# Optimization experiments

Measured on AMD Instinct MI355X. Metric: run time of the kernel, lower is better.

The kernel has to match this reference:

```python
import jax, jax.numpy as jnp
import numpy as np

DIM = 1024
HEADS = 16
HEAD_DIM = DIM // HEADS
HIDDEN = int(DIM * 4.0)
EPS = 1e-5


def layernorm(x, w, b):
    m = jnp.mean(x, axis=-1, keepdims=True)
    v = jnp.var(x, axis=-1, keepdims=True)
    return (x - m) * jax.lax.rsqrt(v + EPS) * w + b


def apply_rope(t, pos):
    # t: [B, H, S, D], pos: [B, S] int
    half = t.shape[-1] // 2
    inv_freq = 1.0 / (10000.0 ** (jnp.arange(half, dtype=jnp.float32) / half))
    ang = pos.astype(jnp.float32)[:, None, :, None] * inv_freq  # [B,1,S,half]
    cos = jnp.cos(ang)
    sin = jnp.sin(ang)
    t1, t2 = t[..., :half], t[..., half:]
    return jnp.concatenate([t1 * cos - t2 * sin, t2 * cos + t1 * sin], axis=-1)


def setup_inputs() -> dict:
    key = jax.random.key(0)
    ks = jax.random.split(key, 10)
    B, S = 2, 2048
    x = jax.random.normal(ks[0], (B, S, DIM), dtype=jnp.float32)
    pos = jnp.sort(jax.random.randint(ks[1], (B, S), 0, 2048), axis=-1).astype(jnp.int32)
    def lin(k, fi, fo):
        return jax.random.normal(k, (fi, fo), dtype=jnp.float32) / np.sqrt(fi)
    return {
        "x": x,
        "pos": pos,
        "ln1_w": jnp.ones((DIM,), jnp.float32),
        "ln1_b": jnp.zeros((DIM,), jnp.float32),
        "qkv_w": lin(ks[2], DIM, 3 * DIM),
        "qkv_b": jnp.zeros((3 * DIM,), jnp.float32),
        "o_w": lin(ks[3], DIM, DIM),
        "o_b": jnp.zeros((DIM,), jnp.float32),
        "ln2_w": jnp.ones((DIM,), jnp.float32),
        "ln2_b": jnp.zeros((DIM,), jnp.float32),
        "mlp_w1": lin(ks[4], DIM, HIDDEN),
        "mlp_b1": jnp.zeros((HIDDEN,), jnp.float32),
        "mlp_w2": lin(ks[5], HIDDEN, DIM),
        "mlp_b2": jnp.zeros((DIM,), jnp.float32),
    }


def reference(x, pos, ln1_w, ln1_b, qkv_w, qkv_b, o_w, o_b, ln2_w, ln2_b, mlp_w1, mlp_b1, mlp_w2, mlp_b2):
    B, S, C = x.shape
    scale = HEAD_DIM ** -0.5
    xn = layernorm(x, ln1_w, ln1_b)
    qkv = (xn @ qkv_w + qkv_b).reshape(B, S, 3, HEADS, HEAD_DIM)
    qkv = jnp.transpose(qkv, (2, 0, 3, 1, 4))  # [3,B,H,S,D]
    q, k, v = qkv[0], qkv[1], qkv[2]
    q = apply_rope(q, pos)
    k = apply_rope(k, pos)
    scores = jnp.einsum("bhsd,bhtd->bhst", q, k) * scale
    probs = jax.nn.softmax(scores, axis=-1)
    attn = jnp.einsum("bhst,bhtd->bhsd", probs, v)
    attn = jnp.transpose(attn, (0, 2, 1, 3)).reshape(B, S, C)
    x = x + attn @ o_w + o_b
    xn2 = layernorm(x, ln2_w, ln2_b)
    h = jax.nn.gelu(xn2 @ mlp_w1 + mlp_b1, approximate=False)
    x = x + h @ mlp_w2 + mlp_b2
    return x
```

## Files before the change

### kernel.cpp

```cpp
#include <hip/hip_runtime.h>
#include <hip/hip_bf16.h>
#include <math.h>

#define DIMC 1024
#define HEADS 16
#define HD 64
#define HIDDEN 4096
#define BATCH 2
#define SEQ 2048
#define TOK (BATCH*SEQ)

typedef unsigned short u16;
typedef __attribute__((ext_vector_type(8))) short short8;
typedef __attribute__((ext_vector_type(4))) float f32x4;

__device__ __forceinline__ u16 f2bf(float f) {
  unsigned u = __float_as_uint(f);
  u += 0x7fff + ((u >> 16) & 1);
  return (u16)(u >> 16);
}
__device__ __forceinline__ float bf2f(u16 h) {
  return __uint_as_float(((unsigned)h) << 16);
}

__device__ __forceinline__ void gl_lds16(const void* g, void* l) {
  __builtin_amdgcn_global_load_lds(
      (__attribute__((address_space(1))) void*)g,
      (__attribute__((address_space(3))) void*)l, 16, 0, 0);
}

__device__ __forceinline__ const short8* lds_row128(const u16* base, int row, int chunk) {
  return (const short8*)((const char*)base + row * 128 + (((chunk) ^ (row & 7)) << 4));
}

__global__ __launch_bounds__(256) void ln_kernel(
    const float* __restrict__ x, const float* __restrict__ w,
    const float* __restrict__ b, u16* __restrict__ out)
{
  int row = blockIdx.x, tid = threadIdx.x;
  const float4* xr = (const float4*)(x + (size_t)row * DIMC);
  float4 v = xr[tid];
  float s = v.x + v.y + v.z + v.w;
  float s2 = v.x*v.x + v.y*v.y + v.z*v.z + v.w*v.w;
  for (int off = 32; off > 0; off >>= 1) {
    s  += __shfl_down(s, off);
    s2 += __shfl_down(s2, off);
  }
  __shared__ float red[8];
  int lane = tid & 63, wv = tid >> 6;
  if (lane == 0) { red[wv] = s; red[4 + wv] = s2; }
  __syncthreads();
  float S  = red[0] + red[1] + red[2] + red[3];
  float S2 = red[4] + red[5] + red[6] + red[7];
  float mean = S * (1.f / DIMC);
  float var  = S2 * (1.f / DIMC) - mean * mean;
  float inv  = rsqrtf(var + 1e-5f);
  int base = tid * 4;
  float vv[4] = {v.x, v.y, v.z, v.w};
#pragma unroll
  for (int j = 0; j < 4; ++j)
    out[(size_t)row * DIMC + base + j] = f2bf((vv[j] - mean) * inv * w[base + j] + b[base + j]);
}

__global__ __launch_bounds__(256) void transpose_cast(
    const float* __restrict__ W, u16* __restrict__ Wt, int K, int N)
{
  __shared__ float t[32][33];
  int n0 = blockIdx.x * 32, k0 = blockIdx.y * 32;
  for (int r = threadIdx.y; r < 32; r += 8)
    t[r][threadIdx.x] = W[(size_t)(k0 + r) * N + n0 + threadIdx.x];
  __syncthreads();
  for (int r = threadIdx.y; r < 32; r += 8)
    Wt[(size_t)(n0 + r) * K + k0 + threadIdx.x] = f2bf(t[threadIdx.x][r]);
}

template<int EPI, int BM>
__global__ __launch_bounds__(256) void gemm_bt(
    const u16* __restrict__ A, const u16* __restrict__ Bt,
    const float* __restrict__ bias, const float* __restrict__ res,
    u16* __restrict__ outb, float* __restrict__ outf,
    int M, int N, int K)
{
  constexpr int AMM = BM / 32;
  constexpr int HALF = BM / 2;
  __shared__ u16 shm[(BM + 128) * 32 * 2];
  u16* As[2] = { shm,             shm + BM * 32 };
  u16* Bs[2] = { shm + 2 * BM * 32, shm + 2 * BM * 32 + 128 * 32 };
  int tid = threadIdx.x;
  int lane = tid & 63, w = tid >> 6;
  int wr = w >> 1, wc = w & 1;

  int nwg = gridDim.x * gridDim.y;
  int orig = blockIdx.y * gridDim.x + blockIdx.x;
  int wg = (orig & 7) * (nwg >> 3) + (orig >> 3);
  int gi = wg >> 4, wi = wg & 15;
  int gx4 = gridDim.x >> 2;
  int bx = (gi % gx4) * 4 + (wi & 3);
  int by = (gi / gx4) * 4 + (wi >> 2);
  int m0 = by * BM, n0 = bx * 128;

  f32x4 acc[AMM][4] = {};

  int trow = tid >> 2;
  int tk = (((tid & 3) ^ ((tid >> 3) & 3)) * 8);
  const u16* ga = A  + (size_t)(m0 + trow) * K + tk;
  const u16* gb = Bt + (size_t)(n0 + trow) * K + tk;
  int rofs = lane & 15, q4 = lane >> 4;
  int ach = ((q4 ^ ((rofs >> 1) & 3)) << 4);
  int nt = K >> 5;

  auto stage = [&](int buf) {
    gl_lds16(ga, As[buf] + tid * 8);
    if (BM == 128) gl_lds16(ga + (size_t)64 * K, As[buf] + tid * 8 + 2048);
    gl_lds16(gb, Bs[buf] + tid * 8);
    gl_lds16(gb + (size_t)64 * K, Bs[buf] + tid * 8 + 2048);
    ga += 32; gb += 32;
  };
  auto compute = [&](int buf) {
    short8 af[AMM], bfr[4];
#pragma unroll
    for (int mm = 0; mm < AMM; ++mm)
      af[mm] = *(const short8*)((const char*)As[buf] + (wr * HALF + mm * 16 + rofs) * 64 + ach);
#pragma unroll
    for (int nn = 0; nn < 4; ++nn)
      bfr[nn] = *(const short8*)((const char*)Bs[buf] + (wc * 64 + nn * 16 + rofs) * 64 + ach);
#pragma unroll
    for (int mm = 0; mm < AMM; ++mm)
#pragma unroll
      for (int nn = 0; nn < 4; ++nn)
        acc[mm][nn] = __builtin_amdgcn_mfma_f32_16x16x32_bf16(af[mm], bfr[nn], acc[mm][nn], 0, 0, 0);
  };

  stage(0);
  __syncthreads();
  for (int t = 0; t < nt; t += 2) {
    if (t + 1 < nt) stage(1);
    compute(0);
    __syncthreads();
    if (t + 2 < nt) stage(0);
    compute(1);
    __syncthreads();
  }

  if (EPI == 0 || EPI == 1) {
    u16* C = shm;
#pragma unroll
    for (int nn = 0; nn < 4; ++nn) {
      int ccol = wc * 64 + nn * 16 + rofs;
      float bv = bias[n0 + ccol];
#pragma unroll
      for (int mm = 0; mm < AMM; ++mm)
#pragma unroll
        for (int r = 0; r < 4; ++r) {
          int crow = wr * HALF + mm * 16 + q4 * 4 + r;
          float v = acc[mm][nn][r] + bv;
          if (EPI == 1) v = 0.5f * v * (1.f + erff(v * 0.70710678118f));
          C[crow * 128 + ccol] = f2bf(v);
        }
    }
    __syncthreads();
    for (int c = tid; c < BM * 16; c += 256) {
      int row = c >> 4, off = (c & 15) * 8;
      *(short8*)(outb + (size_t)(m0 + row) * N + n0 + off) = *(const short8*)&C[row * 128 + off];
    }
  } else {
    float* Cf = (float*)shm;
#pragma unroll
    for (int p = 0; p < 2; ++p) {
      if (wr == p) {
#pragma unroll
        for (int nn = 0; nn < 4; ++nn) {
          int ccol = wc * 64 + nn * 16 + rofs;
          float bv = bias[n0 + ccol];
#pragma unroll
          for (int mm = 0; mm < AMM; ++mm)
#pragma unroll
            for (int r = 0; r < 4; ++r)
              Cf[(mm * 16 + q4 * 4 + r) * 128 + ccol] = acc[mm][nn][r] + bv;
        }
      }
      __syncthreads();
      for (int c = tid; c < HALF * 32; c += 256) {
        int row = c >> 5, off = (c & 31) * 4;
        size_t idx = (size_t)(m0 + p * HALF + row) * N + n0 + off;
        float4 rv = *(const float4*)(res + idx);
        float4 cv = *(const float4*)&Cf[row * 128 + off];
        cv.x += rv.x; cv.y += rv.y; cv.z += rv.z; cv.w += rv.w;
        *(float4*)(outf + idx) = cv;
      }
      __syncthreads();
    }
  }
}

__global__ __launch_bounds__(256) void rope_split(
    const u16* __restrict__ qkv, const int* __restrict__ pos,
    u16* __restrict__ Q, u16* __restrict__ Kk, u16* __restrict__ Vt)
{
  int st = blockIdx.x, bh = blockIdx.y;
  int b = bh >> 4, hh = bh & 15;
  int s0 = st * 64;
  int tid = threadIdx.x;
  __shared__ u16 vtile[64][72];

  for (int i = tid; i < 64 * 32; i += 256) {
    int sl = i >> 5, dp = i & 31;
    int s = s0 + sl;
    float p = (float)pos[b * SEQ + s];
    float freq = exp2f((float)dp * -0.4152410118609203f);
    float ang = p * freq;
    float sn, c;
    __sincosf(ang, &sn, &c);
    const u16* qr = qkv + (size_t)(b * SEQ + s) * 3072 + hh * 64;
    float q1 = bf2f(qr[dp]),        q2 = bf2f(qr[dp + 32]);
    float k1 = bf2f(qr[1024 + dp]), k2 = bf2f(qr[1024 + dp + 32]);
    size_t ob = ((size_t)bh * SEQ + s) * HD;
    const float QS = 0.18033688011112042f;
    Q[ob + dp]       = f2bf((q1 * c - q2 * sn) * QS);
    Q[ob + dp + 32]  = f2bf((q2 * c + q1 * sn) * QS);
    Kk[ob + dp]      = f2bf(k1 * c - k2 * sn);
    Kk[ob + dp + 32] = f2bf(k2 * c + k1 * sn);
  }
  for (int i = tid; i < 64 * 64; i += 256) {
    int sl = i >> 6, d = i & 63;
    vtile[d][sl] = qkv[(size_t)(b * SEQ + s0 + sl) * 3072 + 2048 + hh * 64 + d];
  }
  __syncthreads();
  for (int i = tid; i < 64 * 64; i += 256) {
    int d = i >> 6, sl = i & 63;
    Vt[((size_t)bh * HD + d) * SEQ + s0 + sl] = vtile[d][sl];
  }
}

__global__ __launch_bounds__(256) void attn_kernel(
    const u16* __restrict__ Q, const u16* __restrict__ K,
    const u16* __restrict__ Vt, u16* __restrict__ O)
{
  __shared__ u16 Ks[2][64 * 64];
  __shared__ u16 Vs[2][64 * 64];
  __shared__ u16 Ps[4 * 16 * 64];
  int qt = blockIdx.x, bh = blockIdx.y;
  int b = bh >> 4, hh = bh & 15;
  const u16* Qp = Q + ((size_t)bh * SEQ + qt * 64) * HD;
  const u16* Kp = K + (size_t)bh * SEQ * HD;
  const u16* Vp = Vt + (size_t)bh * HD * SEQ;
  int tid = threadIdx.x, lane = tid & 63, w = tid >> 6;
  int rofs = lane & 15, q4 = lane >> 4;
  int kofs = q4 * 8;

  short8 aq0 = *(const short8*)&Qp[(w * 16 + rofs) * HD + kofs];
  short8 aq1 = *(const short8*)&Qp[(w * 16 + rofs) * HD + 32 + kofs];

  short8 ones;
#pragma unroll
  for (int j = 0; j < 8; ++j) ones[j] = (short)0x3F80;

  f32x4 o[4] = {};
  f32x4 lsum = {};

  int srow = tid >> 3;
  int sg0 = ((tid & 7) ^ (srow & 7)) * 8;
  u16* pw = &Ps[w * 16 * 64];

#define A_STAGE(BUF, T0) do { \
    gl_lds16(Kp + (size_t)((T0) + srow) * HD + sg0, &Ks[BUF][tid * 8]); \
    gl_lds16(Kp + (size_t)((T0) + 32 + srow) * HD + sg0, &Ks[BUF][tid * 8 + 2048]); \
    gl_lds16(Vp + (size_t)srow * SEQ + (T0) + sg0, &Vs[BUF][tid * 8]); \
    gl_lds16(Vp + (size_t)(32 + srow) * SEQ + (T0) + sg0, &Vs[BUF][tid * 8 + 2048]); \
  } while (0)

  auto tile = [&](const u16* KsB, const u16* VsB) {
    f32x4 s[4] = {};
#pragma unroll
    for (int n = 0; n < 4; ++n) {
      int krow = n * 16 + rofs;
      short8 bk0 = *lds_row128(KsB, krow, q4);
      short8 bk1 = *lds_row128(KsB, krow, 4 + q4);
      s[n] = __builtin_amdgcn_mfma_f32_16x16x32_bf16(aq0, bk0, s[n], 0, 0, 0);
      s[n] = __builtin_amdgcn_mfma_f32_16x16x32_bf16(aq1, bk1, s[n], 0, 0, 0);
    }
#pragma unroll
    for (int n = 0; n < 4; ++n)
#pragma unroll
      for (int r = 0; r < 4; ++r) {
        int prow = q4 * 4 + r;
        int pbyte = (n * 16 + rofs) * 2;
        float p = __builtin_amdgcn_exp2f(s[n][r]);
        *(u16*)((char*)pw + prow * 128 + (pbyte ^ ((prow & 7) << 4))) = f2bf(p);
      }
    short8 pa0 = *lds_row128(pw, rofs, q4);
    short8 pa1 = *lds_row128(pw, rofs, 4 + q4);
    lsum = __builtin_amdgcn_mfma_f32_16x16x32_bf16(pa0, ones, lsum, 0, 0, 0);
    lsum = __builtin_amdgcn_mfma_f32_16x16x32_bf16(pa1, ones, lsum, 0, 0, 0);
#pragma unroll
    for (int n = 0; n < 4; ++n) {
      int vrow = n * 16 + rofs;
      short8 bv0 = *lds_row128(VsB, vrow, q4);
      short8 bv1 = *lds_row128(VsB, vrow, 4 + q4);
      o[n] = __builtin_amdgcn_mfma_f32_16x16x32_bf16(pa0, bv0, o[n], 0, 0, 0);
      o[n] = __builtin_amdgcn_mfma_f32_16x16x32_bf16(pa1, bv1, o[n], 0, 0, 0);
    }
  };

  A_STAGE(0, 0);
  __syncthreads();
  for (int t0 = 0; t0 < SEQ; t0 += 128) {
    if (t0 + 64 < SEQ) A_STAGE(1, t0 + 64);
    tile(Ks[0], Vs[0]);
    __syncthreads();
    if (t0 + 128 < SEQ) A_STAGE(0, t0 + 128);
    tile(Ks[1], Vs[1]);
    __syncthreads();
  }
#undef A_STAGE

#pragma unroll
  for (int r = 0; r < 4; ++r) {
    float inv = 1.f / lsum[r];
    int lrow = w * 16 + q4 * 4 + r;
#pragma unroll
    for (int n = 0; n < 4; ++n)
      Ps[lrow * 64 + n * 16 + rofs] = f2bf(o[n][r] * inv);
  }
  __syncthreads();
  for (int c = tid; c < 512; c += 256) {
    int row = c >> 3, off = (c & 7) * 8;
    int sq = qt * 64 + row;
    *(short8*)(O + ((size_t)b * SEQ + sq) * DIMC + hh * 64 + off) = *(const short8*)&Ps[row * 64 + off];
  }
}

extern "C" void kernel_launch(void* const* d_in, const int* in_sizes, int n_in,
                              void* d_out, int out_size, void* d_ws, size_t ws_size,
                              hipStream_t stream) {
  const float* x     = (const float*)d_in[0];
  const int*   pos   = (const int*)  d_in[1];
  const float* ln1_w = (const float*)d_in[2];
  const float* ln1_b = (const float*)d_in[3];
  const float* qkv_w = (const float*)d_in[4];
  const float* qkv_b = (const float*)d_in[5];
  const float* o_w   = (const float*)d_in[6];
  const float* o_b   = (const float*)d_in[7];
  const float* ln2_w = (const float*)d_in[8];
  const float* ln2_b = (const float*)d_in[9];
  const float* w1    = (const float*)d_in[10];
  const float* b1    = (const float*)d_in[11];
  const float* w2    = (const float*)d_in[12];
  const float* b2    = (const float*)d_in[13];
  float* out = (float*)d_out;

  char* ws = (char*)d_ws;
  u16* WqkvT = (u16*)(ws + 0);
  u16* WoT   = (u16*)(ws + 6291456);
  u16* W1T   = (u16*)(ws + 8388608);
  u16* W2T   = (u16*)(ws + 16777216);
  u16* xn    = (u16*)(ws + 25165824);
  u16* qkvbf = (u16*)(ws + 33554432);
  u16* Qb    = (u16*)(ws + 58720256);
  u16* Kb    = (u16*)(ws + 67108864);
  u16* Vtb   = (u16*)(ws + 75497472);
  u16* attnb = (u16*)(ws + 83886080);
  u16* hbuf  = (u16*)(ws + 25165824);
  float* x2  = (float*)(ws + 58720256);
  u16* xn2   = (u16*)(ws + 75497472);

  transpose_cast<<<dim3(3072/32, 1024/32), dim3(32, 8), 0, stream>>>(qkv_w, WqkvT, 1024, 3072);
  transpose_cast<<<dim3(1024/32, 1024/32), dim3(32, 8), 0, stream>>>(o_w,  WoT,  1024, 1024);
  transpose_cast<<<dim3(4096/32, 1024/32), dim3(32, 8), 0, stream>>>(w1,   W1T,  1024, 4096);
  transpose_cast<<<dim3(1024/32, 4096/32), dim3(32, 8), 0, stream>>>(w2,   W2T,  4096, 1024);

  ln_kernel<<<TOK, 256, 0, stream>>>(x, ln1_w, ln1_b, xn);
  gemm_bt<0,128><<<dim3(24, 32), 256, 0, stream>>>(xn, WqkvT, qkv_b, nullptr, qkvbf, nullptr, 4096, 3072, 1024);
  rope_split<<<dim3(32, 32), 256, 0, stream>>>(qkvbf, pos, Qb, Kb, Vtb);
  attn_kernel<<<dim3(32, 32), 256, 0, stream>>>(Qb, Kb, Vtb, attnb);
  gemm_bt<2,64><<<dim3(8, 64), 256, 0, stream>>>(attnb, WoT, o_b, x, nullptr, x2, 4096, 1024, 1024);
  ln_kernel<<<TOK, 256, 0, stream>>>(x2, ln2_w, ln2_b, xn2);
  gemm_bt<1,128><<<dim3(32, 32), 256, 0, stream>>>(xn2, W1T, b1, nullptr, hbuf, nullptr, 4096, 4096, 1024);
  gemm_bt<2,64><<<dim3(8, 64), 256, 0, stream>>>(hbuf, W2T, b2, x2, nullptr, out, 4096, 1024, 4096);
}
```

Before: 268.3 us.

## Add 256x256-tile MFMA GEMM with swizzled LDS and grouped scheduling for QKV and MLP1

Adds a new 512-thread GEMM kernel with 256x256 output tiles, K-step 64, XOR-swizzled LDS staging loaded directly from global memory, and double buffering. It remaps workgroup IDs into 4x4 groups to improve L2 reuse, and stages the output through LDS for coalesced stores. It replaces the 128-row-tile GEMMs for the QKV projection and the first MLP layer. The larger tiles raise arithmetic intensity. In exchange, the grids shrink to 192 and 256 blocks, and the 128KB of LDS per block limits occupancy.

New measurement: 280.6 us. +4.6%, slower.

```diff
diff --git a/kernel.cpp b/kernel.cpp
--- a/kernel.cpp
+++ b/kernel.cpp
@@ -72,6 +72,116 @@
   __syncthreads();
   for (int r = threadIdx.y; r < 32; r += 8)
     Wt[(size_t)(n0 + r) * K + k0 + threadIdx.x] = f2bf(t[threadIdx.x][r]);
+}
+
+template<int EPI>
+__global__ __launch_bounds__(512, 2) void gemm256(
+    const u16* __restrict__ A, const u16* __restrict__ Bt,
+    const float* __restrict__ bias, u16* __restrict__ outb,
+    int M, int N, int K)
+{
+  __shared__ u16 AB[2][2][256 * 64];
+  int tid = threadIdx.x;
+  int lane = tid & 63, wid = tid >> 6;
+  int wr = wid >> 2, wn = wid & 3;
+  int rofs = lane & 15, q4 = lane >> 4;
+
+  int nwg = gridDim.x * gridDim.y;
+  int orig = blockIdx.y * gridDim.x + blockIdx.x;
+  int wg = (orig & 7) * (nwg >> 3) + (orig >> 3);
+  int gi = wg >> 4, wi = wg & 15;
+  int gx4 = gridDim.x >> 2;
+  int bx = (gi % gx4) * 4 + (wi & 3);
+  int by = (gi / gx4) * 4 + (wi >> 2);
+  int m0 = by * 256, n0 = bx * 256;
+  int mb = wr * 128, nb = wn * 64;
+
+  f32x4 acc[8][4] = {};
+
+  int off[4];
+#pragma unroll
+  for (int j = 0; j < 4; ++j) {
+    int p = tid + j * 512;
+    int row = p >> 3;
+    int cl = (p & 7) ^ (row & 7);
+    off[j] = row * K + cl * 8;
+  }
+  const u16* gA = A  + (size_t)m0 * K;
+  const u16* gB = Bt + (size_t)n0 * K;
+
+  auto stage = [&](int b, int t) {
+#pragma unroll
+    for (int j = 0; j < 4; ++j) {
+      int p8 = (tid + j * 512) * 8;
+      gl_lds16(gA + off[j] + t * 64, &AB[b][0][p8]);
+      gl_lds16(gB + off[j] + t * 64, &AB[b][1][p8]);
+    }
+  };
+  auto comp = [&](int b) {
+    const char* Ab = (const char*)&AB[b][0][0];
+    const char* Bb = (const char*)&AB[b][1][0];
+    short8 bf[4][2];
+#pragma unroll
+    for (int nn = 0; nn < 4; ++nn)
+#pragma unroll
+      for (int kk = 0; kk < 2; ++kk) {
+        int row = nb + nn * 16 + rofs;
+        bf[nn][kk] = *(const short8*)(Bb + row * 128 + ((((kk << 2) | q4) ^ (row & 7)) << 4));
+      }
+#pragma unroll
+    for (int mg = 0; mg < 2; ++mg) {
+      short8 af[4][2];
+#pragma unroll
+      for (int mm = 0; mm < 4; ++mm)
+#pragma unroll
+        for (int kk = 0; kk < 2; ++kk) {
+          int row = mb + (mg * 4 + mm) * 16 + rofs;
+          af[mm][kk] = *(const short8*)(Ab + row * 128 + ((((kk << 2) | q4) ^ (row & 7)) << 4));
+        }
+      __builtin_amdgcn_s_setprio(1);
+#pragma unroll
+      for (int kk = 0; kk < 2; ++kk)
+#pragma unroll
+        for (int mm = 0; mm < 4; ++mm)
+#pragma unroll
+          for (int nn = 0; nn < 4; ++nn)
+            acc[mg * 4 + mm][nn] = __builtin_amdgcn_mfma_f32_16x16x32_bf16(
+                af[mm][kk], bf[nn][kk], acc[mg * 4 + mm][nn], 0, 0, 0);
+      __builtin_amdgcn_s_setprio(0);
+    }
+  };
+
+  int NT = K >> 6;
+  stage(0, 0);
+  __syncthreads();
+  int cur = 0;
+  for (int t = 0; t < NT; ++t) {
+    if (t + 1 < NT) stage(cur ^ 1, t + 1);
+    comp(cur);
+    __syncthreads();
+    cur ^= 1;
+  }
+
+  u16* Ct = &AB[0][0][0];
+#pragma unroll
+  for (int nn = 0; nn < 4; ++nn) {
+    int ccol = nb + nn * 16 + rofs;
+    float bv = bias[n0 + ccol];
+#pragma unroll
+    for (int m = 0; m < 8; ++m)
+#pragma unroll
+      for (int r = 0; r < 4; ++r) {
+        int row = mb + m * 16 + q4 * 4 + r;
+        float v = acc[m][nn][r] + bv;
+        if (EPI == 1) v = 0.5f * v * (1.f + erff(v * 0.70710678118f));
+        Ct[row * 256 + ccol] = f2bf(v);
+      }
+  }
+  __syncthreads();
+  for (int c = tid; c < 256 * 32; c += 512) {
+    int row = c >> 5, offb = (c & 31) * 8;
+    *(short8*)(outb + (size_t)(m0 + row) * N + n0 + offb) = *(const short8*)&Ct[row * 256 + offb];
+  }
 }
 
 template<int EPI, int BM>
@@ -370,11 +480,11 @@
   transpose_cast<<<dim3(1024/32, 4096/32), dim3(32, 8), 0, stream>>>(w2,   W2T,  4096, 1024);
 
   ln_kernel<<<TOK, 256, 0, stream>>>(x, ln1_w, ln1_b, xn);
-  gemm_bt<0,128><<<dim3(24, 32), 256, 0, stream>>>(xn, WqkvT, qkv_b, nullptr, qkvbf, nullptr, 4096, 3072, 1024);
+  gemm256<0><<<dim3(12, 16), 512, 0, stream>>>(xn, WqkvT, qkv_b, qkvbf, 4096, 3072, 1024);
   rope_split<<<dim3(32, 32), 256, 0, stream>>>(qkvbf, pos, Qb, Kb, Vtb);
   attn_kernel<<<dim3(32, 32), 256, 0, stream>>>(Qb, Kb, Vtb, attnb);
   gemm_bt<2,64><<<dim3(8, 64), 256, 0, stream>>>(attnb, WoT, o_b, x, nullptr, x2, 4096, 1024, 1024);
   ln_kernel<<<TOK, 256, 0, stream>>>(x2, ln2_w, ln2_b, xn2);
-  gemm_bt<1,128><<<dim3(32, 32), 256, 0, stream>>>(xn2, W1T, b1, nullptr, hbuf, nullptr, 4096, 4096, 1024);
+  gemm256<1><<<dim3(16, 16), 512, 0, stream>>>(xn2, W1T, b1, hbuf, 4096, 4096, 1024);
   gemm_bt<2,64><<<dim3(8, 64), 256, 0, stream>>>(hbuf, W2T, b2, x2, nullptr, out, 4096, 1024, 4096);
 }
```

## Double GEMM K-tile to 64 with 8-chunk XOR swizzle and precomputed offsets

Applied to the files above, without the earlier changes.

The GEMM main loop now stages 64-wide K tiles instead of 32, which halves the number of barrier-separated iterations and doubles the MFMA work between synchronizations. The LDS layout changes to 128-byte rows with an XOR swizzle over 8 chunks, and global load offsets are precomputed per thread. This doubles LDS usage per block, which may reduce occupancy. Offsets are kept as int, which is fine for these sizes.

Result: faster. 256.6 us (-4.3%).

```diff
diff --git a/kernel.cpp b/kernel.cpp
--- a/kernel.cpp
+++ b/kernel.cpp
@@ -81,11 +81,12 @@
     u16* __restrict__ outb, float* __restrict__ outf,
     int M, int N, int K)
 {
-  constexpr int AMM = BM / 32;
+  constexpr int AMM  = BM / 32;
   constexpr int HALF = BM / 2;
-  __shared__ u16 shm[(BM + 128) * 32 * 2];
-  u16* As[2] = { shm,             shm + BM * 32 };
-  u16* Bs[2] = { shm + 2 * BM * 32, shm + 2 * BM * 32 + 128 * 32 };
+  constexpr int AJ   = BM / 32;
+  constexpr int ASZ  = BM * 64;
+  constexpr int BSZ  = 128 * 64;
+  __shared__ u16 shm[(BM + 128) * 64 * 2];
   int tid = threadIdx.x;
   int lane = tid & 63, w = tid >> 6;
   int wr = w >> 1, wc = w & 1;
@@ -101,45 +102,68 @@
 
   f32x4 acc[AMM][4] = {};
 
-  int trow = tid >> 2;
-  int tk = (((tid & 3) ^ ((tid >> 3) & 3)) * 8);
-  const u16* ga = A  + (size_t)(m0 + trow) * K + tk;
-  const u16* gb = Bt + (size_t)(n0 + trow) * K + tk;
+  int offA[AJ], offB[4];
+#pragma unroll
+  for (int j = 0; j < AJ; ++j) {
+    int p = tid + j * 256, row = p >> 3, cl = (p & 7) ^ (row & 7);
+    offA[j] = (m0 + row) * K + cl * 8;
+  }
+#pragma unroll
+  for (int j = 0; j < 4; ++j) {
+    int p = tid + j * 256, row = p >> 3, cl = (p & 7) ^ (row & 7);
+    offB[j] = (n0 + row) * K + cl * 8;
+  }
   int rofs = lane & 15, q4 = lane >> 4;
-  int ach = ((q4 ^ ((rofs >> 1) & 3)) << 4);
-  int nt = K >> 5;
-
-  auto stage = [&](int buf) {
-    gl_lds16(ga, As[buf] + tid * 8);
-    if (BM == 128) gl_lds16(ga + (size_t)64 * K, As[buf] + tid * 8 + 2048);
-    gl_lds16(gb, Bs[buf] + tid * 8);
-    gl_lds16(gb + (size_t)64 * K, Bs[buf] + tid * 8 + 2048);
-    ga += 32; gb += 32;
+  int NT = K >> 6;
+
+  auto stage = [&](int buf, int t) {
+    u16* Ab = shm + buf * ASZ;
+    u16* Bb = shm + 2 * ASZ + buf * BSZ;
+#pragma unroll
+    for (int j = 0; j < AJ; ++j)
+      gl_lds16(A + offA[j] + t * 64, Ab + (tid + j * 256) * 8);
+#pragma unroll
+    for (int j = 0; j < 4; ++j)
+      gl_lds16(Bt + offB[j] + t * 64, Bb + (tid + j * 256) * 8);
   };
   auto compute = [&](int buf) {
-    short8 af[AMM], bfr[4];
+    const char* Ab = (const char*)(shm + buf * ASZ);
+    const char* Bb = (const char*)(shm + 2 * ASZ + buf * BSZ);
+    short8 af[AMM][2], bfr[4][2];
 #pragma unroll
     for (int mm = 0; mm < AMM; ++mm)
-      af[mm] = *(const short8*)((const char*)As[buf] + (wr * HALF + mm * 16 + rofs) * 64 + ach);
+#pragma unroll
+      for (int kk = 0; kk < 2; ++kk) {
+        int row = wr * HALF + mm * 16 + rofs;
+        af[mm][kk] = *(const short8*)(Ab + row * 128 +
+                                      ((((kk << 2) | q4) ^ (row & 7)) << 4));
+      }
 #pragma unroll
     for (int nn = 0; nn < 4; ++nn)
-      bfr[nn] = *(const short8*)((const char*)Bs[buf] + (wc * 64 + nn * 16 + rofs) * 64 + ach);
-#pragma unroll
-    for (int mm = 0; mm < AMM; ++mm)
-#pragma unroll
-      for (int nn = 0; nn < 4; ++nn)
-        acc[mm][nn] = __builtin_amdgcn_mfma_f32_16x16x32_bf16(af[mm], bfr[nn], acc[mm][nn], 0, 0, 0);
+#pragma unroll
+      for (int kk = 0; kk < 2; ++kk) {
+        int row = wc * 64 + nn * 16 + rofs;
+        bfr[nn][kk] = *(const short8*)(Bb + row * 128 +
+                                       ((((kk << 2) | q4) ^ (row & 7)) << 4));
+      }
+#pragma unroll
+    for (int kk = 0; kk < 2; ++kk)
+#pragma unroll
+      for (int mm = 0; mm < AMM; ++mm)
+#pragma unroll
+        for (int nn = 0; nn < 4; ++nn)
+          acc[mm][nn] = __builtin_amdgcn_mfma_f32_16x16x32_bf16(
+              af[mm][kk], bfr[nn][kk], acc[mm][nn], 0, 0, 0);
   };
 
-  stage(0);
-  __syncthreads();
-  for (int t = 0; t < nt; t += 2) {
-    if (t + 1 < nt) stage(1);
-    compute(0);
+  stage(0, 0);
+  __syncthreads();
+  int cur = 0;
+  for (int t = 0; t < NT; ++t) {
+    if (t + 1 < NT) stage(cur ^ 1, t + 1);
+    compute(cur);
     __syncthreads();
-    if (t + 2 < nt) stage(0);
-    compute(1);
-    __syncthreads();
+    cur ^= 1;
   }
 
   if (EPI == 0 || EPI == 1) {
```
